# Performance work log

Measured on AMD Instinct MI355X. Metric: run time of the kernel, lower is better.

## Reference

```python
import jax, jax.numpy as jnp
import numpy as np

K = 1024          # number of breakpoints in the LUT
N_ROWS = 4096
N_COLS = 16384


def setup_inputs() -> dict:
    key = jax.random.key(0)
    k1, k2, k3, k4 = jax.random.split(key, 4)
    # Breakpoints must be sorted for the LUT semantics (sum(d > x) == searchsorted).
    x = jnp.sort(jax.random.normal(k1, (K,), dtype=jnp.float32) * 3.0)
    a = jax.random.normal(k2, (K + 1,), dtype=jnp.float32)  # per-segment slope
    b = jax.random.normal(k3, (K + 1,), dtype=jnp.float32)  # per-segment intercept
    data = jax.random.normal(k4, (N_ROWS, N_COLS), dtype=jnp.float32)
    return {"data": data, "x": x, "a": a, "b": b}


def reference(data, x, a, b):
    # Original: index = sum(d > x_i) over breakpoints. With x sorted ascending this
    # equals the number of breakpoints strictly less than d, i.e.
    # searchsorted(x, d, side='left'). This avoids the [N, K] compare matrix.
    d = data.reshape(-1)
    index = jnp.searchsorted(x, d, side="left")  # int32 in [0, K]
    out = a[index] * d + b[index]                 # gather + FMA, one pass
    return out.reshape(data.shape)
```

## Files before the change

kernel.cpp:

```cpp
#include <hip/hip_runtime.h>


#define LUT_K 1024
#define XPAD (LUT_K + (LUT_K / 32))

__device__ __forceinline__ int swiz(int i) { return i + (i >> 5); }

__global__ __launch_bounds__(256) void lut_kernel(
    const float* __restrict__ data, const float* __restrict__ x,
    const float* __restrict__ a, const float* __restrict__ b,
    float* __restrict__ out, int n4)
{
    __shared__ float xs[XPAD];
    __shared__ float2 ab[LUT_K + 1];

    for (int i = threadIdx.x; i < LUT_K; i += blockDim.x)
        xs[swiz(i)] = x[i];
    for (int i = threadIdx.x; i < LUT_K + 1; i += blockDim.x)
        ab[i] = make_float2(a[i], b[i]);
    __syncthreads();

    const float4* __restrict__ in4 = (const float4*)data;
    float4* __restrict__ out4 = (float4*)out;

    auto eval = [&](float v) -> float {
        int pos = 0;
        #pragma unroll
        for (int s = 512; s > 0; s >>= 1)
            pos += (xs[swiz(pos + s - 1)] < v) ? s : 0;
        pos += (xs[swiz(pos)] < v) ? 1 : 0;
        float2 c = ab[pos];
        return fmaf(c.x, v, c.y);
    };

    const int stride = gridDim.x * blockDim.x;
    for (int i = blockIdx.x * blockDim.x + threadIdx.x; i < n4; i += stride) {
        float4 d = in4[i];
        float4 r;
        r.x = eval(d.x);
        r.y = eval(d.y);
        r.z = eval(d.z);
        r.w = eval(d.w);
        out4[i] = r;
    }
}

extern "C" void kernel_launch(void* const* d_in, const int* in_sizes, int n_in,
                              void* d_out, int out_size, void* d_ws, size_t ws_size,
                              hipStream_t stream) {
    const float* data = (const float*)d_in[0];
    const float* x    = (const float*)d_in[1];
    const float* a    = (const float*)d_in[2];
    const float* b    = (const float*)d_in[3];
    float* out = (float*)d_out;

    int n  = in_sizes[0];
    int n4 = n >> 2;

    dim3 block(256);
    dim3 grid(2048);
    lut_kernel<<<grid, block, 0, stream>>>(data, x, a, b, out, n4);
}
```

Baseline: 453.8 us.

## Replace per-element binary search with uniform-bucket index table plus linear scan

```diff
diff --git a/kernel.cpp b/kernel.cpp
--- a/kernel.cpp
+++ b/kernel.cpp
@@ -2,35 +2,80 @@
 
 
 #define LUT_K 1024
-#define XPAD (LUT_K + (LUT_K / 32))
+#define NB    8192
+#define WS_NEEDED (NB * 2 + 8)
 
-__device__ __forceinline__ int swiz(int i) { return i + (i >> 5); }
+__device__ __forceinline__ int bucket_of(float v, float x0, float invw) {
+    int t = (int)__fmul_rn(__fsub_rn(v, x0), invw);
+    t = t < 0 ? 0 : t;
+    return t > (NB - 1) ? (NB - 1) : t;
+}
 
-__global__ __launch_bounds__(256) void lut_kernel(
+__global__ __launch_bounds__(256) void build_kernel(const float* __restrict__ x, void* ws) {
+    __shared__ float xs[LUT_K];
+    unsigned short* bs = (unsigned short*)ws;
+    float* params = (float*)((char*)ws + NB * 2);
+    for (int i = threadIdx.x; i < LUT_K; i += blockDim.x) xs[i] = x[i];
+    __syncthreads();
+    const float x0 = xs[0];
+    const float invw = (float)NB / (xs[LUT_K - 1] - x0);
+    if (blockIdx.x == 0 && threadIdx.x == 0) { params[0] = x0; params[1] = invw; }
+    int j = blockIdx.x * blockDim.x + threadIdx.x;
+    if (j < NB) {
+        int lo = 0, hi = LUT_K;
+        while (lo < hi) {
+            int mid = (lo + hi) >> 1;
+            if (bucket_of(xs[mid], x0, invw) < j) lo = mid + 1; else hi = mid;
+        }
+        bs[j] = (unsigned short)lo;
+    }
+}
+
+__global__ __launch_bounds__(256) void lut_main(
     const float* __restrict__ data, const float* __restrict__ x,
     const float* __restrict__ a, const float* __restrict__ b,
-    float* __restrict__ out, int n4)
+    const void* __restrict__ ws, float* __restrict__ out, int n4, int use_ws)
 {
-    __shared__ float xs[XPAD];
-    __shared__ float2 ab[LUT_K + 1];
+    __shared__ float xs[LUT_K + 1];
+    __shared__ float aa[LUT_K + 1];
+    __shared__ float bb[LUT_K + 1];
+    __shared__ __align__(16) unsigned short bs[NB];
 
-    for (int i = threadIdx.x; i < LUT_K; i += blockDim.x)
-        xs[swiz(i)] = x[i];
-    for (int i = threadIdx.x; i < LUT_K + 1; i += blockDim.x)
-        ab[i] = make_float2(a[i], b[i]);
-    __syncthreads();
+    for (int i = threadIdx.x; i < LUT_K; i += blockDim.x) xs[i] = x[i];
+    for (int i = threadIdx.x; i < LUT_K + 1; i += blockDim.x) { aa[i] = a[i]; bb[i] = b[i]; }
+    if (threadIdx.x == 0) xs[LUT_K] = __builtin_inff();
+
+    float x0, invw;
+    if (use_ws) {
+        const float* params = (const float*)((const char*)ws + NB * 2);
+        x0 = params[0]; invw = params[1];
+        const uint2* gbs = (const uint2*)ws;
+        for (int i = threadIdx.x; i < NB / 4; i += blockDim.x)
+            ((uint2*)bs)[i] = gbs[i];
+        __syncthreads();
+    } else {
+        __syncthreads();
+        x0 = xs[0];
+        invw = (float)NB / (xs[LUT_K - 1] - x0);
+        for (int j = threadIdx.x; j < NB; j += blockDim.x) {
+            int lo = 0, hi = LUT_K;
+            while (lo < hi) {
+                int mid = (lo + hi) >> 1;
+                if (bucket_of(xs[mid], x0, invw) < j) lo = mid + 1; else hi = mid;
+            }
+            bs[j] = (unsigned short)lo;
+        }
+        __syncthreads();
+    }
 
     const float4* __restrict__ in4 = (const float4*)data;
     float4* __restrict__ out4 = (float4*)out;
 
     auto eval = [&](float v) -> float {
-        int pos = 0;
-        #pragma unroll
-        for (int s = 512; s > 0; s >>= 1)
-            pos += (xs[swiz(pos + s - 1)] < v) ? s : 0;
-        pos += (xs[swiz(pos)] < v) ? 1 : 0;
-        float2 c = ab[pos];
-        return fmaf(c.x, v, c.y);
+        int j = bucket_of(v, x0, invw);
+        int idx = bs[j];
+        while (xs[idx] < v) idx++;
+        return fmaf(aa[idx], v, bb[idx]);
     };
 
     const int stride = gridDim.x * blockDim.x;
@@ -57,7 +102,9 @@
     int n  = in_sizes[0];
     int n4 = n >> 2;
 
-    dim3 block(256);
-    dim3 grid(2048);
-    lut_kernel<<<grid, block, 0, stream>>>(data, x, a, b, out, n4);
+    int use_ws = (ws_size >= (size_t)WS_NEEDED) ? 1 : 0;
+    if (use_ws)
+        build_kernel<<<(NB + 255) / 256, 256, 0, stream>>>(x, d_ws);
+
+    lut_main<<<1280, 256, 0, stream>>>(data, x, a, b, d_ws, out, n4, use_ws);
 }
```

Result: faster. 439.6 us (-3.1%).
